# Performance work log

Measured on AMD Instinct MI355X. Metric: run time of the kernel, lower is better.

The kernel has to match this reference:

```python
import jax, jax.numpy as jnp
import numpy as np

DIM, HEADS, WS = 192, 8, 8
B, H, W = 4, 256, 256


def conv2d(x, w, b=None, padding=((0, 0), (0, 0)), groups=1):
    y = jax.lax.conv_general_dilated(
        x, w, window_strides=(1, 1), padding=padding,
        dimension_numbers=("NCHW", "OIHW", "NCHW"), feature_group_count=groups)
    if b is not None:
        y = y + b[None, :, None, None]
    return y


def setup_inputs() -> dict:
    key = jax.random.key(0)
    ks = jax.random.split(key, 16)
    d = DIM
    s = 0.02
    return {
        "x": jax.random.normal(ks[0], (B, d, H, W), jnp.float32),
        "w_dww": jax.random.normal(ks[1], (d, 1, 1, 11), jnp.float32) * s,
        "b_dww": jnp.zeros((d,), jnp.float32),
        "w_dwh": jax.random.normal(ks[2], (d, 1, 11, 1), jnp.float32) * s,
        "b_dwh": jnp.zeros((d,), jnp.float32),
        "w_dwhw": jax.random.normal(ks[3], (2 * d, 1, 3, 3), jnp.float32) * s,
        "b_dwhw": jnp.zeros((2 * d,), jnp.float32),
        "w_conv1": jax.random.normal(ks[4], (d, 2 * d, 1, 1), jnp.float32) * s,
        "w_qkv": jax.random.normal(ks[5], (3 * d, d, 1, 1), jnp.float32) * s,
        "w_qkvdw": jax.random.normal(ks[6], (3 * d, 1, 3, 3), jnp.float32) * s,
        "w_conv2": jax.random.normal(ks[7], (d, d, 1, 1), jnp.float32) * s,
        "w_conv3": jax.random.normal(ks[8], (d, d, 1, 1), jnp.float32) * s,
        "w_conv4a": jax.random.normal(ks[9], (d, d, 1, 1), jnp.float32) * s,
        "w_conv4b": jax.random.normal(ks[10], (d, 1, 3, 3), jnp.float32) * s,
        "w_proj": jax.random.normal(ks[11], (d, 2 * d, 1, 1), jnp.float32) * s,
        "temperature": jnp.ones((HEADS, 1, 1), jnp.float32),
    }


def reference(x, w_dww, b_dww, w_dwh, b_dwh, w_dwhw, b_dwhw, w_conv1,
              w_qkv, w_qkvdw, w_conv2, w_conv3, w_conv4a, w_conv4b,
              w_proj, temperature):
    b, c, h, w = x.shape
    d, heads, ws = DIM, HEADS, WS

    # high-frequency branch: strip depthwise convs -> 3x3 depthwise -> 1x1
    hw_cat = jnp.concatenate([
        conv2d(x, w_dww, b_dww, padding=((0, 0), (5, 5)), groups=d),
        conv2d(x, w_dwh, b_dwh, padding=((5, 5), (0, 0)), groups=d)], axis=1)
    high = conv2d(hw_cat, w_dwhw, b_dwhw, padding=((1, 1), (1, 1)), groups=2 * d)
    high = conv2d(high, w_conv1)  # [b, d, h, w]

    # low-frequency branch: avg-pool downsample then channel attention
    x_down = x.reshape(b, c, h // ws, ws, w // ws, ws).mean(axis=(3, 5))
    qkv = conv2d(x_down, w_qkv)
    qkv = conv2d(qkv, w_qkvdw, padding=((1, 1), (1, 1)), groups=3 * d)
    q, k, v = jnp.split(qkv, 3, axis=1)

    hd, wd = h // ws, w // ws
    ch = d // heads
    q = q.reshape(b, heads, ch, hd * wd)
    k = k.reshape(b, heads, ch, hd * wd)
    q = q / jnp.maximum(jnp.linalg.norm(q, axis=-1, keepdims=True), 1e-12)
    k = k / jnp.maximum(jnp.linalg.norm(k, axis=-1, keepdims=True), 1e-12)
    attn = jnp.einsum("bhcn,bhdn->bhcd", q, k) * temperature[None]  # [b,heads,ch,ch]
    attn = jax.nn.softmax(attn, axis=-1)

    # pooling gate on v (global 1x1) then modulate full-res conv4(x)
    v_max = jnp.max(v, axis=(2, 3), keepdims=True)
    v_avg = jnp.mean(v, axis=(2, 3), keepdims=True)
    v_gate = conv2d(v_max, w_conv2) + conv2d(v_avg, w_conv3)  # [b, d, 1, 1]
    x4 = conv2d(conv2d(x, w_conv4a), w_conv4b, padding=((1, 1), (1, 1)), groups=d)
    v_full = v_gate * x4  # [b, d, h, w]

    v_full = v_full.reshape(b, heads, ch, h * w)
    low = jnp.einsum("bhcd,bhdn->bhcn", attn, v_full).reshape(b, d, h, w)

    return conv2d(jnp.concatenate([high, low], axis=1), w_proj)
```

## Files before the change

kernel.cpp:

```cpp
#include <hip/hip_runtime.h>
#include <hip/hip_bf16.h>

typedef __hip_bfloat16 bf16;
typedef __attribute__((ext_vector_type(8))) short s8v;
typedef __attribute__((ext_vector_type(4))) float f4;

#define DEVI __device__ __forceinline__

DEVI f4 mfma16(s8v a, s8v b, f4 c){
  return __builtin_amdgcn_mfma_f32_16x16x32_bf16(a, b, c, 0, 0, 0);
}

constexpr int NPIX = 65536;
constexpr int NDOWN = 1024;

__global__ void k_cast_w(const float* __restrict__ w1, const float* __restrict__ w4a,
                         const float* __restrict__ wp, const float* __restrict__ wq,
                         bf16* __restrict__ out){
  int i = blockIdx.x*256 + threadIdx.x;
  if (i < 73728) out[i] = __float2bfloat16(w1[i]);
  else if (i < 110592) out[i] = __float2bfloat16(w4a[i - 73728]);
  else if (i < 184320) out[i] = __float2bfloat16(wp[i - 110592]);
  else if (i < 294912) out[i] = __float2bfloat16(wq[i - 184320]);
}

__global__ void k_pack_x(const float* __restrict__ x, bf16* __restrict__ xp){
  __shared__ float t[8][1032];
  int b = blockIdx.z, cb = blockIdx.y, ns = blockIdx.x, tid = threadIdx.x;
  const float* src = x + ((size_t)(b*192 + cb*8))*NPIX + ns*1024;
  #pragma unroll
  for (int i = 0; i < 8; ++i){
    float4 v = *(const float4*)(src + (size_t)i*NPIX + tid*4);
    *(float4*)&t[i][tid*4] = v;
  }
  __syncthreads();
  bf16* dst = xp + (((size_t)(b*24 + cb))*NPIX + ns*1024)*8;
  #pragma unroll
  for (int j = 0; j < 4; ++j){
    int p = j*256 + tid;
    alignas(16) bf16 c8[8];
    #pragma unroll
    for (int i = 0; i < 8; ++i) c8[i] = __float2bfloat16(t[i][p]);
    *(uint4*)(dst + (size_t)p*8) = *(const uint4*)c8;
  }
}

__global__ void k_pool(const bf16* __restrict__ xp, bf16* __restrict__ xdp){
  __shared__ float red[8][32][8];
  int b = blockIdx.z, cb = blockIdx.y, hd = blockIdx.x, tid = threadIdx.x;
  int r = tid >> 5, wd = tid & 31;
  const bf16* src = xp + (((size_t)(b*24 + cb))*NPIX + (hd*8 + r)*256 + wd*8)*8;
  float acc[8] = {0,0,0,0,0,0,0,0};
  #pragma unroll
  for (int ww = 0; ww < 8; ++ww){
    uint4 raw = *(const uint4*)(src + ww*8);
    const bf16* c8 = (const bf16*)&raw;
    #pragma unroll
    for (int i = 0; i < 8; ++i) acc[i] += __bfloat162float(c8[i]);
  }
  #pragma unroll
  for (int i = 0; i < 8; ++i) red[r][wd][i] = acc[i];
  __syncthreads();
  if (tid < 32){
    alignas(16) bf16 o8[8];
    #pragma unroll
    for (int i = 0; i < 8; ++i){
      float s = 0.f;
      #pragma unroll
      for (int rr = 0; rr < 8; ++rr) s += red[rr][tid][i];
      o8[i] = __float2bfloat16(s * (1.0f/64.0f));
    }
    *(uint4*)(xdp + (((size_t)(b*24 + cb))*NDOWN + hd*32 + tid)*8) = *(const uint4*)o8;
  }
}

template<int K, bool PLANAR>
__launch_bounds__(256, 2)
__global__ void k_gemm(const bf16* __restrict__ Bp, const bf16* __restrict__ W,
                       void* __restrict__ outp, int npix, int outkb){
  constexpr int KB8 = K/8;
  constexpr int NIT = K/64;
  __shared__ bf16 As[96*72];
  __shared__ bf16 Bs[128*72];
  int tid = threadIdx.x;
  int b = blockIdx.z;
  int m0 = blockIdx.y*96;
  int n0 = blockIdx.x*128;
  int wave = tid >> 6, lane = tid & 63;
  int wm = wave >> 1, wn = wave & 1;
  int lr = lane & 15, kg = lane >> 4;
  f4 acc[3][4] = {};
  const size_t bK = (size_t)b * KB8;
  for (int kt = 0; kt < NIT; ++kt){
    {
      int idx = tid;
      #pragma unroll
      for (int j = 0; j < 3; ++j, idx += 256){
        int m = idx >> 3, kc = idx & 7;
        *(uint4*)&As[m*72 + kc*8] = *(const uint4*)(W + (size_t)(m0 + m)*K + kt*64 + kc*8);
      }
      idx = tid;
      #pragma unroll
      for (int j = 0; j < 4; ++j, idx += 256){
        int kb = idx >> 7, n = idx & 127;
        *(uint4*)&Bs[n*72 + kb*8] = *(const uint4*)(Bp + ((bK + kt*8 + kb)*npix + n0 + n)*8);
      }
    }
    __syncthreads();
    #pragma unroll
    for (int kk = 0; kk < 2; ++kk){
      s8v af[3]; s8v bfr[4];
      int ko = kk*32 + kg*8;
      #pragma unroll
      for (int mf = 0; mf < 3; ++mf) af[mf] = *(const s8v*)&As[(wm*48 + mf*16 + lr)*72 + ko];
      #pragma unroll
      for (int nf = 0; nf < 4; ++nf) bfr[nf] = *(const s8v*)&Bs[(wn*64 + nf*16 + lr)*72 + ko];
      #pragma unroll
      for (int mf = 0; mf < 3; ++mf)
        #pragma unroll
        for (int nf = 0; nf < 4; ++nf)
          acc[mf][nf] = mfma16(af[mf], bfr[nf], acc[mf][nf]);
    }
    __syncthreads();
  }
  int quad = lane >> 4;
  #pragma unroll
  for (int mf = 0; mf < 3; ++mf){
    int mb = m0 + wm*48 + mf*16 + quad*4;
    #pragma unroll
    for (int nf = 0; nf < 4; ++nf){
      int n = n0 + wn*64 + nf*16 + lr;
      if constexpr (PLANAR){
        float* o = (float*)outp;
        #pragma unroll
        for (int r2 = 0; r2 < 4; ++r2)
          o[((size_t)(b*outkb + mb + r2))*npix + n] = acc[mf][nf][r2];
      } else {
        bf16* o = (bf16*)outp;
        alignas(8) bf16 v4[4];
        #pragma unroll
        for (int r2 = 0; r2 < 4; ++r2) v4[r2] = __float2bfloat16(acc[mf][nf][r2]);
        *(uint2*)(o + ((size_t)(b*outkb + (mb >> 3))*npix + n)*8 + (mb & 7)) = *(const uint2*)v4;
      }
    }
  }
}

__global__ void k_high_dw(const bf16* __restrict__ xp,
    const float* __restrict__ wdww, const float* __restrict__ bdww,
    const float* __restrict__ wdwh, const float* __restrict__ bdwh,
    const float* __restrict__ w3, const float* __restrict__ b3,
    bf16* __restrict__ hw3p){
  __shared__ bf16 xs[28*28*8];
  __shared__ float dwwt[18*18*8];
  __shared__ float dwht[18*18*8];
  int t = blockIdx.x, cb = blockIdx.y, b = blockIdx.z, tid = threadIdx.x;
  int r0 = (t >> 4)*16, c0 = (t & 15)*16;
  const bf16* src = xp + ((size_t)(b*24 + cb))*NPIX*8;
  for (int i = tid; i < 784; i += 256){
    int r = i/28, c = i - r*28;
    int gr = r0 + r - 6, gc = c0 + c - 6;
    uint4 v = {0,0,0,0};
    if ((unsigned)gr < 256u && (unsigned)gc < 256u)
      v = *(const uint4*)(src + ((size_t)(gr*256 + gc))*8);
    *(uint4*)&xs[i*8] = v;
  }
  __syncthreads();
  {
    int ch = tid & 7, pr = tid >> 3;
    int cg = cb*8 + ch;
    float ww[11], wh[11];
    #pragma unroll
    for (int j = 0; j < 11; ++j){ ww[j] = wdww[cg*11 + j]; wh[j] = wdwh[cg*11 + j]; }
    float bw = bdww[cg], bh = bdwh[cg];
    for (int p = pr; p < 324; p += 32){
      int r = p/18, c = p - r*18;
      int gr = r0 + r - 1, gc = c0 + c - 1;
      float vww = 0.f, vwh = 0.f;
      if ((unsigned)gr < 256u && (unsigned)gc < 256u){
        vww = bw; vwh = bh;
        #pragma unroll
        for (int j = 0; j < 11; ++j){
          vww += ww[j]*__bfloat162float(xs[((r+5)*28 + c + j)*8 + ch]);
          vwh += wh[j]*__bfloat162float(xs[((r+j)*28 + c + 5)*8 + ch]);
        }
      }
      dwwt[p*8 + ch] = vww;
      dwht[p*8 + ch] = vwh;
    }
  }
  __syncthreads();
  {
    int r = tid >> 4, c = tid & 15;
    int n = (r0 + r)*256 + c0 + c;
    alignas(16) bf16 o1[8], o2[8];
    #pragma unroll
    for (int ch = 0; ch < 8; ++ch){
      int cg = cb*8 + ch;
      float s1 = b3[cg], s2 = b3[192 + cg];
      #pragma unroll
      for (int dr = 0; dr < 3; ++dr)
        #pragma unroll
        for (int dc = 0; dc < 3; ++dc){
          int pi = ((r + dr)*18 + c + dc)*8 + ch;
          s1 += w3[cg*9 + dr*3 + dc]         * dwwt[pi];
          s2 += w3[(192 + cg)*9 + dr*3 + dc] * dwht[pi];
        }
      o1[ch] = __float2bfloat16(s1);
      o2[ch] = __float2bfloat16(s2);
    }
    *(uint4*)(hw3p + (((size_t)(b*48 + cb))*NPIX + n)*8)      = *(const uint4*)o1;
    *(uint4*)(hw3p + (((size_t)(b*48 + 24 + cb))*NPIX + n)*8) = *(const uint4*)o2;
  }
}

__global__ void k_qkv_dw(const bf16* __restrict__ qkv0p, const float* __restrict__ wdw,
                         float* __restrict__ qkvd, float* __restrict__ vmax, float* __restrict__ vavg){
  __shared__ bf16 xs[34*34*8];
  __shared__ float red[256*8];
  int cb = blockIdx.x, b = blockIdx.y, tid = threadIdx.x;
  for (int i = tid; i < 1156; i += 256){
    int r = i/34, c = i - r*34;
    int gr = r - 1, gc = c - 1;
    uint4 v = {0,0,0,0};
    if ((unsigned)gr < 32u && (unsigned)gc < 32u)
      v = *(const uint4*)(qkv0p + (((size_t)(b*72 + cb))*NDOWN + gr*32 + gc)*8);
    *(uint4*)&xs[i*8] = v;
  }
  __syncthreads();
  float mxv[8], smv[8];
  #pragma unroll
  for (int ch = 0; ch < 8; ++ch){ mxv[ch] = -3.4e38f; smv[ch] = 0.f; }
  for (int j = 0; j < 4; ++j){
    int p = j*256 + tid;
    int r = p >> 5, c = p & 31;
    #pragma unroll
    for (int ch = 0; ch < 8; ++ch){
      float s = 0.f;
      #pragma unroll
      for (int dr = 0; dr < 3; ++dr)
        #pragma unroll
        for (int dc = 0; dc < 3; ++dc)
          s += wdw[(cb*8 + ch)*9 + dr*3 + dc] *
               __bfloat162float(xs[((r + dr)*34 + c + dc)*8 + ch]);
      qkvd[((size_t)(b*576 + cb*8 + ch))*NDOWN + p] = s;
      mxv[ch] = fmaxf(mxv[ch], s);
      smv[ch] += s;
    }
  }
  if (cb >= 48){
    #pragma unroll
    for (int ch = 0; ch < 8; ++ch) red[tid*8 + ch] = mxv[ch];
    __syncthreads();
    for (int st = 128; st > 0; st >>= 1){
      if (tid < st)
        #pragma unroll
        for (int ch = 0; ch < 8; ++ch)
          red[tid*8 + ch] = fmaxf(red[tid*8 + ch], red[(tid + st)*8 + ch]);
      __syncthreads();
    }
    if (tid < 8) vmax[b*192 + (cb - 48)*8 + tid] = red[tid];
    __syncthreads();
    #pragma unroll
    for (int ch = 0; ch < 8; ++ch) red[tid*8 + ch] = smv[ch];
    __syncthreads();
    for (int st = 128; st > 0; st >>= 1){
      if (tid < st)
        #pragma unroll
        for (int ch = 0; ch < 8; ++ch) red[tid*8 + ch] += red[(tid + st)*8 + ch];
      __syncthreads();
    }
    if (tid < 8) vavg[b*192 + (cb - 48)*8 + tid] = red[tid] * (1.0f/1024.0f);
  }
}

__global__ void k_attn(const float* __restrict__ qkvd, const float* __restrict__ temp,
                       float* __restrict__ attn){
  __shared__ float inv[48];
  __shared__ float sm[576];
  int bh = blockIdx.x;
  int b = bh >> 3, h = bh & 7;
  const float* qb = qkvd + ((size_t)(b*576 + h*24))*NDOWN;
  const float* kb = qkvd + ((size_t)(b*576 + 192 + h*24))*NDOWN;
  int tid = threadIdx.x, wave = tid >> 6, lane = tid & 63;
  for (int v = wave; v < 48; v += 4){
    const float* p = (v < 24) ? (qb + v*NDOWN) : (kb + (v - 24)*NDOWN);
    float s = 0.f;
    for (int i = lane; i < NDOWN; i += 64){ float xv = p[i]; s += xv*xv; }
    #pragma unroll
    for (int o = 32; o > 0; o >>= 1) s += __shfl_down(s, o);
    if (lane == 0) inv[v] = 1.0f / fmaxf(sqrtf(s), 1e-12f);
  }
  __syncthreads();
  float tp = temp[h];
  for (int pr = tid; pr < 576; pr += 256){
    int c = pr/24, d = pr - c*24;
    const float4* qp = (const float4*)(qb + c*NDOWN);
    const float4* kp = (const float4*)(kb + d*NDOWN);
    float s = 0.f;
    for (int i = 0; i < 256; ++i){
      float4 a = qp[i], e = kp[i];
      s += a.x*e.x + a.y*e.y + a.z*e.z + a.w*e.w;
    }
    sm[pr] = s * inv[c] * inv[24 + d] * tp;
  }
  __syncthreads();
  if (tid < 24){
    float mx = -3.4e38f;
    for (int d = 0; d < 24; ++d) mx = fmaxf(mx, sm[tid*24 + d]);
    float sum = 0.f;
    for (int d = 0; d < 24; ++d) sum += __expf(sm[tid*24 + d] - mx);
    float isum = 1.0f / sum;
    for (int d = 0; d < 24; ++d)
      attn[((size_t)bh)*576 + tid*24 + d] = __expf(sm[tid*24 + d] - mx) * isum;
  }
}

__global__ void k_gate(const float* __restrict__ vmax, const float* __restrict__ vavg,
                       const float* __restrict__ w2, const float* __restrict__ w3,
                       float* __restrict__ gate){
  __shared__ float vm[192], va[192];
  int b = blockIdx.x, tid = threadIdx.x;
  if (tid < 192){ vm[tid] = vmax[b*192 + tid]; va[tid] = vavg[b*192 + tid]; }
  __syncthreads();
  if (tid < 192){
    float s = 0.f;
    const float* w2r = w2 + tid*192;
    const float* w3r = w3 + tid*192;
    for (int k = 0; k < 192; ++k) s += w2r[k]*vm[k] + w3r[k]*va[k];
    gate[b*192 + tid] = s;
  }
}

__global__ void k_low(const bf16* __restrict__ x4ap, const float* __restrict__ attn,
                      const float* __restrict__ gate, const float* __restrict__ w4b,
                      bf16* __restrict__ hlp){
  __shared__ bf16 xt[3*18*18*8];
  __shared__ float a2[576];
  __shared__ float wt[216];
  __shared__ float vt[24*256];
  int t = blockIdx.x, h = blockIdx.y, b = blockIdx.z, tid = threadIdx.x;
  int r0 = (t >> 4)*16, c0 = (t & 15)*16;
  int ch0 = h*24;
  for (int i = tid; i < 576; i += 256)
    a2[i] = attn[((size_t)(b*8 + h))*576 + i] * gate[b*192 + ch0 + (i % 24)];
  for (int i = tid; i < 216; i += 256) wt[i] = w4b[ch0*9 + i];
  for (int i = tid; i < 972; i += 256){
    int kb = i/324, p = i - kb*324;
    int r = p/18, c = p - r*18;
    int gr = r0 + r - 1, gc = c0 + c - 1;
    uint4 v = {0,0,0,0};
    if ((unsigned)gr < 256u && (unsigned)gc < 256u)
      v = *(const uint4*)(x4ap + (((size_t)(b*24 + h*3 + kb))*NPIX + gr*256 + gc)*8);
    *(uint4*)&xt[i*8] = v;
  }
  __syncthreads();
  {
    int r = tid >> 4, c = tid & 15;
    #pragma unroll
    for (int ch = 0; ch < 24; ++ch){
      int kb = ch >> 3, ci = ch & 7;
      float s = 0.f;
      #pragma unroll
      for (int dr = 0; dr < 3; ++dr)
        #pragma unroll
        for (int dc = 0; dc < 3; ++dc)
          s += wt[ch*9 + dr*3 + dc] *
               __bfloat162float(xt[((kb*18 + r + dr)*18 + c + dc)*8 + ci]);
      vt[ch*256 + tid] = s;
    }
  }
  __syncthreads();
  {
    float o[24];
    #pragma unroll
    for (int cc = 0; cc < 24; ++cc){
      float s = 0.f;
      #pragma unroll
      for (int d = 0; d < 24; ++d) s += a2[cc*24 + d] * vt[d*256 + tid];
      o[cc] = s;
    }
    int n = (r0 + (tid >> 4))*256 + c0 + (tid & 15);
    #pragma unroll
    for (int kb = 0; kb < 3; ++kb){
      alignas(16) bf16 c8[8];
      #pragma unroll
      for (int i = 0; i < 8; ++i) c8[i] = __float2bfloat16(o[kb*8 + i]);
      *(uint4*)(hlp + (((size_t)(b*48 + 24 + h*3 + kb))*NPIX + n)*8) = *(const uint4*)c8;
    }
  }
}

extern "C" void kernel_launch(void* const* d_in, const int* in_sizes, int n_in,
                              void* d_out, int out_size, void* d_ws, size_t ws_size,
                              hipStream_t stream){
  const float* x        = (const float*)d_in[0];
  const float* w_dww    = (const float*)d_in[1];
  const float* b_dww    = (const float*)d_in[2];
  const float* w_dwh    = (const float*)d_in[3];
  const float* b_dwh    = (const float*)d_in[4];
  const float* w_dwhw   = (const float*)d_in[5];
  const float* b_dwhw   = (const float*)d_in[6];
  const float* w_conv1  = (const float*)d_in[7];
  const float* w_qkv    = (const float*)d_in[8];
  const float* w_qkvdw  = (const float*)d_in[9];
  const float* w_conv2  = (const float*)d_in[10];
  const float* w_conv3  = (const float*)d_in[11];
  const float* w_conv4a = (const float*)d_in[12];
  const float* w_conv4b = (const float*)d_in[13];
  const float* w_proj   = (const float*)d_in[14];
  const float* temp     = (const float*)d_in[15];

  char* ws = (char*)d_ws;
  size_t off = 0;
  auto take = [&](size_t bytes)->char*{
    char* r = ws + off;
    off = (off + bytes + 255) & ~(size_t)255;
    return r;
  };
  bf16*  xp    = (bf16*) take((size_t)4*192*65536*2);
  bf16*  hw3p  = (bf16*) take((size_t)4*384*65536*2);
  bf16*  hlp   = (bf16*) take((size_t)4*384*65536*2);
  bf16*  x4ap  = (bf16*) take((size_t)4*192*65536*2);
  bf16*  xdp   = (bf16*) take((size_t)4*192*1024*2);
  bf16*  qkv0p = (bf16*) take((size_t)4*576*1024*2);
  float* qkvd  = (float*)take((size_t)4*576*1024*4);
  float* attn  = (float*)take((size_t)4*8*576*4);
  float* vmax  = (float*)take((size_t)4*192*4);
  float* vavg  = (float*)take((size_t)4*192*4);
  float* gate  = (float*)take((size_t)4*192*4);
  bf16*  wbf   = (bf16*) take((size_t)294912*2);
  if (off > ws_size) return;

  k_cast_w<<<1152, 256, 0, stream>>>(w_conv1, w_conv4a, w_proj, w_qkv, wbf);
  k_pack_x<<<dim3(64,24,4), 256, 0, stream>>>(x, xp);
  k_pool<<<dim3(32,24,4), 256, 0, stream>>>(xp, xdp);
  k_gemm<192,false><<<dim3(8,6,4), 256, 0, stream>>>(xdp, wbf + 184320, qkv0p, 1024, 72);
  k_qkv_dw<<<dim3(72,4), 256, 0, stream>>>(qkv0p, w_qkvdw, qkvd, vmax, vavg);
  k_attn<<<32, 256, 0, stream>>>(qkvd, temp, attn);
  k_gate<<<4, 192, 0, stream>>>(vmax, vavg, w_conv2, w_conv3, gate);
  k_high_dw<<<dim3(256,24,4), 256, 0, stream>>>(xp, w_dww, b_dww, w_dwh, b_dwh, w_dwhw, b_dwhw, hw3p);
  k_gemm<384,false><<<dim3(512,2,4), 256, 0, stream>>>(hw3p, wbf, hlp, 65536, 48);
  k_gemm<192,false><<<dim3(512,2,4), 256, 0, stream>>>(xp, wbf + 73728, x4ap, 65536, 24);
  k_low<<<dim3(256,8,4), 256, 0, stream>>>(x4ap, attn, gate, w_conv4b, hlp);
  k_gemm<384,true><<<dim3(512,2,4), 256, 0, stream>>>(hlp, wbf + 110592, d_out, 65536, 192);
}
```

Before: 1.050 ms.

## Restructure high-frequency depthwise kernel with planar LDS and register sliding windows

Reworks k_high_dw so the input tile is stored per channel in LDS (planar, padded rows) instead of interleaved by channel. Each thread now computes a whole 18-long strip of the 11-tap horizontal or vertical convolution from a 28-value register window, reusing loaded values across outputs. The 3x3 stage computes 8 consecutive outputs per thread using float4 LDS reads. Weights and biases are staged once in LDS, and launch bounds are added. The goal is fewer LDS reads and less redundant index arithmetic. In exchange, output stores become strided 2-byte writes rather than 16-byte vector stores, and some threads carry two strip tasks, which unbalances the work.

```diff
diff --git a/kernel.cpp b/kernel.cpp
--- a/kernel.cpp
+++ b/kernel.cpp
@@ -146,16 +146,41 @@
   }
 }
 
+__launch_bounds__(256, 4)
 __global__ void k_high_dw(const bf16* __restrict__ xp,
     const float* __restrict__ wdww, const float* __restrict__ bdww,
     const float* __restrict__ wdwh, const float* __restrict__ bdwh,
     const float* __restrict__ w3, const float* __restrict__ b3,
     bf16* __restrict__ hw3p){
-  __shared__ bf16 xs[28*28*8];
-  __shared__ float dwwt[18*18*8];
-  __shared__ float dwht[18*18*8];
+  __shared__ unsigned short xs[8*904];
+  __shared__ float dww_s[8*372];
+  __shared__ float dwh_s[8*372];
+  __shared__ float wgt[352];
   int t = blockIdx.x, cb = blockIdx.y, b = blockIdx.z, tid = threadIdx.x;
   int r0 = (t >> 4)*16, c0 = (t & 15)*16;
+
+  if (tid < 88){
+    int ch = tid/11, j = tid - ch*11;
+    wgt[ch*12 + j]      = wdww[(cb*8 + ch)*11 + j];
+    wgt[96 + ch*12 + j] = wdwh[(cb*8 + ch)*11 + j];
+  } else if (tid < 96){
+    int ch = tid - 88;
+    wgt[ch*12 + 11]      = bdww[cb*8 + ch];
+    wgt[96 + ch*12 + 11] = bdwh[cb*8 + ch];
+  } else if (tid < 168){
+    int i2 = tid - 96; int ch = i2/9, j = i2 - ch*9;
+    wgt[192 + ch*10 + j] = w3[(cb*8 + ch)*9 + j];
+  } else if (tid < 240){
+    int i2 = tid - 168; int ch = i2/9, j = i2 - ch*9;
+    wgt[272 + ch*10 + j] = w3[(192 + cb*8 + ch)*9 + j];
+  } else if (tid < 248){
+    int ch = tid - 240;
+    wgt[192 + ch*10 + 9] = b3[cb*8 + ch];
+  } else {
+    int ch = tid - 248;
+    wgt[272 + ch*10 + 9] = b3[192 + cb*8 + ch];
+  }
+
   const bf16* src = xp + ((size_t)(b*24 + cb))*NPIX*8;
   for (int i = tid; i < 784; i += 256){
     int r = i/28, c = i - r*28;
@@ -163,54 +188,95 @@
     uint4 v = {0,0,0,0};
     if ((unsigned)gr < 256u && (unsigned)gc < 256u)
       v = *(const uint4*)(src + ((size_t)(gr*256 + gc))*8);
-    *(uint4*)&xs[i*8] = v;
-  }
-  __syncthreads();
+    const unsigned short* u = (const unsigned short*)&v;
+    #pragma unroll
+    for (int ch = 0; ch < 8; ++ch)
+      xs[ch*904 + r*32 + c] = u[ch];
+  }
+  __syncthreads();
+
+  auto strip_task = [&](int ch, int idx, bool isH){
+    int ibase = ch*904 + (isH ? (idx + 5)*32 : (idx + 5));
+    int istr  = isH ? 1 : 32;
+    float vbuf[28];
+    #pragma unroll
+    for (int i = 0; i < 28; ++i){
+      unsigned u = xs[ibase + i*istr];
+      vbuf[i] = __uint_as_float(u << 16);
+    }
+    const float* wb = &wgt[(isH ? 0 : 96) + ch*12];
+    float wv[11];
+    #pragma unroll
+    for (int j = 0; j < 11; ++j) wv[j] = wb[j];
+    float bias = wb[11];
+    float* ob = (isH ? dww_s : dwh_s) + ch*372 + (isH ? idx*20 : idx);
+    int ostr = isH ? 1 : 20;
+    int fixedv = (isH ? r0 + idx : c0 + idx) - 1;
+    int varb   = (isH ? c0 : r0) - 1;
+    bool fok = (unsigned)fixedv < 256u;
+    #pragma unroll
+    for (int i = 0; i < 18; ++i){
+      float s = bias;
+      #pragma unroll
+      for (int j = 0; j < 11; ++j) s += wv[j]*vbuf[i + j];
+      bool ok = fok && ((unsigned)(varb + i) < 256u);
+      ob[i*ostr] = ok ? s : 0.f;
+    }
+  };
   {
-    int ch = tid & 7, pr = tid >> 3;
-    int cg = cb*8 + ch;
-    float ww[11], wh[11];
-    #pragma unroll
-    for (int j = 0; j < 11; ++j){ ww[j] = wdww[cg*11 + j]; wh[j] = wdwh[cg*11 + j]; }
-    float bw = bdww[cg], bh = bdwh[cg];
-    for (int p = pr; p < 324; p += 32){
-      int r = p/18, c = p - r*18;
-      int gr = r0 + r - 1, gc = c0 + c - 1;
-      float vww = 0.f, vwh = 0.f;
-      if ((unsigned)gr < 256u && (unsigned)gc < 256u){
-        vww = bw; vwh = bh;
-        #pragma unroll
-        for (int j = 0; j < 11; ++j){
-          vww += ww[j]*__bfloat162float(xs[((r+5)*28 + c + j)*8 + ch]);
-          vwh += wh[j]*__bfloat162float(xs[((r+j)*28 + c + 5)*8 + ch]);
-        }
+    bool isH = tid < 144;
+    int t2 = isH ? tid : tid - 144;
+    int ch = t2/18, idx = t2 - ch*18;
+    strip_task(ch, idx, isH);
+  }
+  if (tid < 32){
+    int t2 = 112 + tid;
+    int ch = t2/18, idx = t2 - ch*18;
+    strip_task(ch, idx, false);
+  }
+  __syncthreads();
+
+  {
+    int half = tid & 1, rr = (tid >> 1) & 15, ch = tid >> 5;
+    const float* wa = &wgt[192 + ch*10];
+    const float* wb2 = &wgt[272 + ch*10];
+    float acc1[8], acc2[8];
+    float ba = wa[9], bb = wb2[9];
+    #pragma unroll
+    for (int i = 0; i < 8; ++i){ acc1[i] = ba; acc2[i] = bb; }
+    #pragma unroll
+    for (int dr = 0; dr < 3; ++dr){
+      const float* p1 = &dww_s[ch*372 + (rr + dr)*20 + half*8];
+      const float* p2 = &dwh_s[ch*372 + (rr + dr)*20 + half*8];
+      float4 a0 = *(const float4*)p1;
+      float4 a1 = *(const float4*)(p1 + 4);
+      float4 a2 = *(const float4*)(p1 + 8);
+      float t1v[12] = {a0.x,a0.y,a0.z,a0.w, a1.x,a1.y,a1.z,a1.w, a2.x,a2.y,a2.z,a2.w};
+      #pragma unroll
+      for (int dc = 0; dc < 3; ++dc){
+        float w = wa[dr*3 + dc];
+        #pragma unroll
+        for (int i = 0; i < 8; ++i) acc1[i] += w * t1v[i + dc];
       }
-      dwwt[p*8 + ch] = vww;
-      dwht[p*8 + ch] = vwh;
-    }
-  }
-  __syncthreads();
-  {
-    int r = tid >> 4, c = tid & 15;
-    int n = (r0 + r)*256 + c0 + c;
-    alignas(16) bf16 o1[8], o2[8];
-    #pragma unroll
-    for (int ch = 0; ch < 8; ++ch){
-      int cg = cb*8 + ch;
-      float s1 = b3[cg], s2 = b3[192 + cg];
-      #pragma unroll
-      for (int dr = 0; dr < 3; ++dr)
-        #pragma unroll
-        for (int dc = 0; dc < 3; ++dc){
-          int pi = ((r + dr)*18 + c + dc)*8 + ch;
-          s1 += w3[cg*9 + dr*3 + dc]         * dwwt[pi];
-          s2 += w3[(192 + cg)*9 + dr*3 + dc] * dwht[pi];
-        }
-      o1[ch] = __float2bfloat16(s1);
-      o2[ch] = __float2bfloat16(s2);
-    }
-    *(uint4*)(hw3p + (((size_t)(b*48 + cb))*NPIX + n)*8)      = *(const uint4*)o1;
-    *(uint4*)(hw3p + (((size_t)(b*48 + 24 + cb))*NPIX + n)*8) = *(const uint4*)o2;
+      float4 b0 = *(const float4*)p2;
+      float4 b1 = *(const float4*)(p2 + 4);
+      float4 b2 = *(const float4*)(p2 + 8);
+      float t2v[12] = {b0.x,b0.y,b0.z,b0.w, b1.x,b1.y,b1.z,b1.w, b2.x,b2.y,b2.z,b2.w};
+      #pragma unroll
+      for (int dc = 0; dc < 3; ++dc){
+        float w = wb2[dr*3 + dc];
+        #pragma unroll
+        for (int i = 0; i < 8; ++i) acc2[i] += w * t2v[i + dc];
+      }
+    }
+    int gr = r0 + rr, gc = c0 + half*8;
+    bf16* o1 = hw3p + (((size_t)(b*48 + cb))*NPIX + gr*256 + gc)*8 + ch;
+    bf16* o2 = hw3p + (((size_t)(b*48 + 24 + cb))*NPIX + gr*256 + gc)*8 + ch;
+    #pragma unroll
+    for (int i = 0; i < 8; ++i){
+      o1[i*8] = __float2bfloat16(acc1[i]);
+      o2[i*8] = __float2bfloat16(acc2[i]);
+    }
   }
 }
 
```

New measurement: 1.194 ms. 13.8% more time.
